# Kernel tuning notes

Measured on AMD Instinct MI355X. Metric: run time of the kernel, lower is better.

## Reference

```python
import jax, jax.numpy as jnp
import numpy as np

EPS = 1e-5

def _ln(x, g, b):
    mu = jnp.mean(x, axis=-1, keepdims=True)
    var = jnp.mean((x - mu) ** 2, axis=-1, keepdims=True)
    return (x - mu) * jax.lax.rsqrt(var + EPS) * g + b

def _lin(x, W, b):
    return x @ W + b

def setup_inputs() -> dict:
    B, D_IN, H = 32768, 512, 512
    key = jax.random.key(0)
    ks = jax.random.split(key, 20)
    def W(k, din, dout):
        return jax.random.normal(k, (din, dout), jnp.float32) / np.sqrt(din)
    inp = {
        'x': jax.random.normal(ks[0], (B, D_IN), jnp.float32),
        'h_prev': jax.random.normal(ks[1], (B, H), jnp.float32),
        's_prev': jax.random.normal(ks[2], (B, H), jnp.float32),
        'W_in': W(ks[3], D_IN, H), 'b_in': jnp.zeros((H,), jnp.float32),
        'g_ln_in': jnp.ones((H,), jnp.float32), 'b_ln_in': jnp.zeros((H,), jnp.float32),
        'g_ln_r': jnp.ones((H,), jnp.float32), 'b_ln_r': jnp.zeros((H,), jnp.float32),
        'g_ln_z': jnp.ones((H,), jnp.float32), 'b_ln_z': jnp.zeros((H,), jnp.float32),
        'g_ln_h': jnp.ones((H,), jnp.float32), 'b_ln_h': jnp.zeros((H,), jnp.float32),
        'W_r': W(ks[4], H, H), 'b_r': jnp.zeros((H,), jnp.float32),
        'W_z': W(ks[5], H, H), 'b_z': jnp.zeros((H,), jnp.float32),
        'W_k': W(ks[6], H, H), 'b_k': jnp.zeros((H,), jnp.float32),
        'W_v': W(ks[7], H, H), 'b_v': jnp.zeros((H,), jnp.float32),
        'W_h': W(ks[8], H, H), 'b_h': jnp.zeros((H,), jnp.float32),
        'W_d': W(ks[9], H, H), 'b_d': jnp.zeros((H,), jnp.float32),
    }
    return inp

def reference(x, h_prev, s_prev, W_in, b_in, g_ln_in, b_ln_in,
              g_ln_r, b_ln_r, g_ln_z, b_ln_z, g_ln_h, b_ln_h,
              W_r, b_r, W_z, b_z, W_k, b_k, W_v, b_v, W_h, b_h, W_d, b_d):
    # u = LN(input_proj(x))
    u = _ln(_lin(x, W_in, b_in), g_ln_in, b_ln_in)
    r = jax.nn.sigmoid(_ln(_lin(u, W_r, b_r), g_ln_r, b_ln_r))  # computed as in original (unused downstream)
    z = jax.nn.sigmoid(_ln(_lin(u, W_z, b_z), g_ln_z, b_ln_z))
    k = _lin(u, W_k, b_k)
    v = _lin(u, W_v, b_v)
    decay = jax.nn.sigmoid(_lin(u, W_d, b_d))
    s = decay * s_prev + k * v
    c = jnp.tanh(_ln(_lin(u + s, W_h, b_h), g_ln_h, b_ln_h))
    h = (1.0 - z) * c + z * h_prev
    return (h, s)
```

## Files before the change

### kernel.cpp

```cpp
#include <hip/hip_runtime.h>

typedef __attribute__((ext_vector_type(8))) short bf16x8;
typedef __attribute__((ext_vector_type(4))) float f32x4;

#define LN_EPS 1e-5f
#define MSZ ((size_t)32768 * 512)
#define WSZ ((size_t)512 * 512)

typedef const __attribute__((address_space(1))) void* gptr_t;
typedef __attribute__((address_space(3))) void* lptr_t;

__device__ __forceinline__ float b2f(unsigned short h) {
    unsigned int u = ((unsigned int)h) << 16;
    return __uint_as_float(u);
}
__device__ __forceinline__ short f2b(float f) {
    unsigned int u = __float_as_uint(f);
    unsigned int r = (u + 0x7FFFu + ((u >> 16) & 1u)) >> 16;
    return (short)(unsigned short)r;
}
__device__ __forceinline__ float sigmoid_f(float x) {
    return 1.0f / (1.0f + __expf(-x));
}
__device__ __forceinline__ float ldS(const void* p, size_t i, int isbf) {
    return isbf ? b2f(((const unsigned short*)p)[i]) : ((const float*)p)[i];
}
__device__ __forceinline__ void ld8(const void* p, size_t i, int isbf, float* o) {
    if (isbf) {
        bf16x8 v = *(const bf16x8*)((const unsigned short*)p + i);
        #pragma unroll
        for (int j = 0; j < 8; ++j) o[j] = b2f((unsigned short)v[j]);
    } else {
        f32x4 a = *(const f32x4*)((const float*)p + i);
        f32x4 b = *(const f32x4*)((const float*)p + i + 4);
        #pragma unroll
        for (int j = 0; j < 4; ++j) { o[j] = a[j]; o[4 + j] = b[j]; }
    }
}

__global__ void detect_dtype(const unsigned int* __restrict__ ones, int* __restrict__ flag) {
    if (threadIdx.x == 0 && blockIdx.x == 0)
        *flag = (ones[0] == 0x3F803F80u) ? 1 : 0;
}

__global__ __launch_bounds__(256) void transpose6(
    const void* __restrict__ s0, const void* __restrict__ s1,
    const void* __restrict__ s2, const void* __restrict__ s3,
    const void* __restrict__ s4, const void* __restrict__ s5,
    unsigned short* __restrict__ d0, unsigned short* __restrict__ d1,
    unsigned short* __restrict__ d2, unsigned short* __restrict__ d3,
    unsigned short* __restrict__ d4, unsigned short* __restrict__ d5,
    const int* __restrict__ flagp)
{
    const int isbf = *flagp;
    const void* srcs[6] = {s0, s1, s2, s3, s4, s5};
    unsigned short* dsts[6] = {d0, d1, d2, d3, d4, d5};
    const void* src = srcs[blockIdx.z];
    unsigned short* dst = dsts[blockIdx.z];

    __shared__ unsigned short tile[32][33];
    int tx = threadIdx.x, ty = threadIdx.y;
    int colbase = blockIdx.x * 32;
    int rowbase = blockIdx.y * 32;
    #pragma unroll
    for (int i = 0; i < 32; i += 8)
        tile[ty + i][tx] = (unsigned short)f2b(
            ldS(src, (size_t)(rowbase + ty + i) * 512 + colbase + tx, isbf));
    __syncthreads();
    #pragma unroll
    for (int i = 0; i < 32; i += 8)
        dst[(size_t)(colbase + ty + i) * 512 + rowbase + tx] = tile[tx][ty + i];
}

template<int OUT, bool CONV>
__global__ __launch_bounds__(512) void gemm_row(
    const void* __restrict__ Araw,
    const unsigned short* __restrict__ BT,
    const void* __restrict__ bias,
    const void* __restrict__ g0, const void* __restrict__ b0v,
    const void* __restrict__ g1, const void* __restrict__ b1v,
    const unsigned short* __restrict__ zlin,
    const void* __restrict__ h_prev,
    void* __restrict__ out,
    const int* __restrict__ flagp)
{
    const int isbf = *flagp;
    const int K = 512;
    __shared__ unsigned short smem[36864];
    unsigned short* As = smem;
    unsigned short* Bs = smem + 64 * 64;

    int t = threadIdx.x;
    int lane = t & 63;
    int wave = t >> 6;
    int wn = wave * 64;

    int b = blockIdx.x;
    int m0 = ((b & 7) * 64 + (b >> 3)) * 64;

    int lr = lane >> 3, lg = lane & 7, gsrc = lg ^ lr;
    const unsigned short* Ab = (const unsigned short*)Araw;

    size_t a_off = (size_t)(m0 + 8 * wave + lr) * K + gsrc * 8;
    size_t b_off[8];
    #pragma unroll
    for (int i = 0; i < 8; ++i)
        b_off[i] = (size_t)(64 * wave + 8 * i + lr) * K + gsrc * 8;

    int cr = t >> 3, cg = t & 7;

    int ml = lane & 15, kg = lane >> 4, sw = ml & 7;

    f32x4 acc[4][4] = {};
    const bool conv_now = CONV && !isbf;

    for (int k0 = 0; k0 < K; k0 += 64) {
        if (conv_now) {
            const float* Af = (const float*)Araw;
            size_t gi = (size_t)(m0 + cr) * K + k0 + cg * 8;
            f32x4 lo = *(const f32x4*)&Af[gi];
            f32x4 hi = *(const f32x4*)&Af[gi + 4];
            bf16x8 p;
            #pragma unroll
            for (int z = 0; z < 4; ++z) { p[z] = f2b(lo[z]); p[4 + z] = f2b(hi[z]); }
            *(bf16x8*)&As[cr * 64 + ((cg ^ (cr & 7)) * 8)] = p;
        } else {
            __builtin_amdgcn_global_load_lds(
                (gptr_t)(const void*)(Ab + a_off + k0),
                (lptr_t)(void*)(As + wave * 512), 16, 0, 0);
        }
        #pragma unroll
        for (int i = 0; i < 8; ++i)
            __builtin_amdgcn_global_load_lds(
                (gptr_t)(const void*)(BT + b_off[i] + k0),
                (lptr_t)(void*)(Bs + (wave * 8 + i) * 512), 16, 0, 0);
        __syncthreads();

        #pragma unroll
        for (int ks = 0; ks < 2; ++ks) {
            int ga = ((ks << 2) + kg) ^ sw;
            bf16x8 af[4], bfr[4];
            #pragma unroll
            for (int i = 0; i < 4; ++i)
                af[i] = *(const bf16x8*)&As[(i * 16 + ml) * 64 + ga * 8];
            #pragma unroll
            for (int j = 0; j < 4; ++j)
                bfr[j] = *(const bf16x8*)&Bs[(wn + j * 16 + ml) * 64 + ga * 8];
            #pragma unroll
            for (int i = 0; i < 4; ++i)
                #pragma unroll
                for (int j = 0; j < 4; ++j)
                    acc[i][j] = __builtin_amdgcn_mfma_f32_16x16x32_bf16(
                        af[i], bfr[j], acc[i][j], 0, 0, 0);
        }
        __syncthreads();
    }

    unsigned short* E = smem;
    int cq = lane >> 4, cl = lane & 15;
    #pragma unroll
    for (int j = 0; j < 4; ++j) {
        float bv = ldS(bias, wn + j * 16 + cl, isbf);
        #pragma unroll
        for (int i = 0; i < 4; ++i)
            #pragma unroll
            for (int r = 0; r < 4; ++r)
                E[(i * 16 + cq * 4 + r) * 520 + wn + j * 16 + cl] =
                    (unsigned short)f2b(acc[i][j][r] + bv);
    }
    __syncthreads();

    if (OUT == 0) {
        float gv[8], bv[8];
        ld8(g0, (size_t)lane * 8, isbf, gv);
        ld8(b0v, (size_t)lane * 8, isbf, bv);
        #pragma unroll
        for (int q = 0; q < 8; ++q) {
            int r = wave * 8 + q;
            bf16x8 xv = *(const bf16x8*)&E[r * 520 + lane * 8];
            float x[8], s = 0.f, s2 = 0.f;
            #pragma unroll
            for (int i = 0; i < 8; ++i) {
                x[i] = b2f((unsigned short)xv[i]);
                s += x[i]; s2 += x[i] * x[i];
            }
            #pragma unroll
            for (int off = 32; off > 0; off >>= 1) {
                s += __shfl_xor(s, off); s2 += __shfl_xor(s2, off);
            }
            float mu = s * (1.f / 512.f);
            float rs = rsqrtf(s2 * (1.f / 512.f) - mu * mu + LN_EPS);
            bf16x8 o;
            #pragma unroll
            for (int i = 0; i < 8; ++i)
                o[i] = f2b((x[i] - mu) * rs * gv[i] + bv[i]);
            *(bf16x8*)&((unsigned short*)out)[(size_t)(m0 + r) * 512 + lane * 8] = o;
        }
    } else {
        float gh[8], bh[8], gz[8], bz[8];
        ld8(g0, (size_t)lane * 8, isbf, gh);
        ld8(b0v, (size_t)lane * 8, isbf, bh);
        ld8(g1, (size_t)lane * 8, isbf, gz);
        ld8(b1v, (size_t)lane * 8, isbf, bz);
        #pragma unroll
        for (int q = 0; q < 8; ++q) {
            int r = wave * 8 + q;
            size_t base = (size_t)(m0 + r) * 512 + lane * 8;
            bf16x8 hv8 = *(const bf16x8*)&E[r * 520 + lane * 8];
            bf16x8 zv8 = *(const bf16x8*)&zlin[base];
            float hf[8], zf[8];
            float sh = 0.f, sh2 = 0.f, sz = 0.f, sz2 = 0.f;
            #pragma unroll
            for (int i = 0; i < 8; ++i) {
                hf[i] = b2f((unsigned short)hv8[i]);
                zf[i] = b2f((unsigned short)zv8[i]);
                sh += hf[i]; sh2 += hf[i] * hf[i];
                sz += zf[i]; sz2 += zf[i] * zf[i];
            }
            #pragma unroll
            for (int off = 32; off > 0; off >>= 1) {
                sh += __shfl_xor(sh, off); sh2 += __shfl_xor(sh2, off);
                sz += __shfl_xor(sz, off); sz2 += __shfl_xor(sz2, off);
            }
            float muh = sh * (1.f / 512.f);
            float rsh = rsqrtf(sh2 * (1.f / 512.f) - muh * muh + LN_EPS);
            float muz = sz * (1.f / 512.f);
            float rsz = rsqrtf(sz2 * (1.f / 512.f) - muz * muz + LN_EPS);
            float hp[8];
            ld8(h_prev, base, isbf, hp);
            float hout[8];
            #pragma unroll
            for (int i = 0; i < 8; ++i) {
                float z = sigmoid_f((zf[i] - muz) * rsz * gz[i] + bz[i]);
                float c = tanhf((hf[i] - muh) * rsh * gh[i] + bh[i]);
                hout[i] = (1.f - z) * c + z * hp[i];
            }
            if (isbf) {
                bf16x8 o;
                #pragma unroll
                for (int i = 0; i < 8; ++i) o[i] = f2b(hout[i]);
                *(bf16x8*)&((unsigned short*)out)[base] = o;
            } else {
                f32x4 lo, hi;
                #pragma unroll
                for (int i = 0; i < 4; ++i) { lo[i] = hout[i]; hi[i] = hout[4 + i]; }
                *(f32x4*)&((float*)out)[base] = lo;
                *(f32x4*)&((float*)out)[base + 4] = hi;
            }
        }
    }
}

__global__ __launch_bounds__(256) void gemm_zkvd(
    const unsigned short* __restrict__ U,
    const unsigned short* __restrict__ BT,
    const void* __restrict__ bz, const void* __restrict__ bk,
    const void* __restrict__ bv_, const void* __restrict__ bd,
    const void* __restrict__ s_prev,
    unsigned short* __restrict__ zout,
    unsigned short* __restrict__ aout,
    void* __restrict__ dout,
    const int* __restrict__ flagp)
{
    const int isbf = *flagp;
    const int K = 512;
    __shared__ unsigned short smem[20480];
    unsigned short* As = smem;

    int t = threadIdx.x;
    int lane = t & 63;
    int wave = t >> 6;
    int wm = (wave >> 1) * 32;
    int wn = (wave & 1) * 32;

    int b = blockIdx.x;
    int xcd = b & 7;
    int bi = b >> 3;
    int nb = bi & 7;
    int mi = bi >> 3;
    int m0 = (xcd * 64 + mi) * 64;
    int nc0 = nb * 64;

    int lr = lane >> 3, lg = lane & 7, gsrc = lg ^ lr;

    size_t a_off[2], b_off[8];
    #pragma unroll
    for (int i = 0; i < 2; ++i)
        a_off[i] = (size_t)(m0 + 8 * (2 * wave + i) + lr) * K + gsrc * 8;
    #pragma unroll
    for (int i = 0; i < 8; ++i)
        b_off[i] = (size_t)(wave * 512 + nc0 + 8 * i + lr) * K + gsrc * 8;

    int ml = lane & 15, kg = lane >> 4, sw = ml & 7;

    f32x4 acc[4][2][2] = {};

    for (int k0 = 0; k0 < K; k0 += 64) {
        #pragma unroll
        for (int i = 0; i < 2; ++i)
            __builtin_amdgcn_global_load_lds(
                (gptr_t)(const void*)(U + a_off[i] + k0),
                (lptr_t)(void*)(As + (2 * wave + i) * 512), 16, 0, 0);
        #pragma unroll
        for (int i = 0; i < 8; ++i)
            __builtin_amdgcn_global_load_lds(
                (gptr_t)(const void*)(BT + b_off[i] + k0),
                (lptr_t)(void*)(smem + 4096 + wave * 4096 + i * 512), 16, 0, 0);
        __syncthreads();

        #pragma unroll
        for (int ks = 0; ks < 2; ++ks) {
            int ga = ((ks << 2) + kg) ^ sw;
            bf16x8 af[2];
            #pragma unroll
            for (int i = 0; i < 2; ++i)
                af[i] = *(const bf16x8*)&As[(wm + i * 16 + ml) * 64 + ga * 8];
            #pragma unroll
            for (int s = 0; s < 4; ++s) {
                bf16x8 bf0 = *(const bf16x8*)&smem[4096 + s * 4096 + (wn + ml) * 64 + ga * 8];
                bf16x8 bf1 = *(const bf16x8*)&smem[4096 + s * 4096 + (wn + 16 + ml) * 64 + ga * 8];
                #pragma unroll
                for (int i = 0; i < 2; ++i) {
                    acc[s][i][0] = __builtin_amdgcn_mfma_f32_16x16x32_bf16(
                        af[i], bf0, acc[s][i][0], 0, 0, 0);
                    acc[s][i][1] = __builtin_amdgcn_mfma_f32_16x16x32_bf16(
                        af[i], bf1, acc[s][i][1], 0, 0, 0);
                }
            }
        }
        __syncthreads();
    }

    int cq = lane >> 4, cl = lane & 15;
    const void* biases[4] = {bz, bk, bv_, bd};
    #pragma unroll
    for (int s = 0; s < 4; ++s) {
        #pragma unroll
        for (int j = 0; j < 2; ++j) {
            float bvv = ldS(biases[s], nc0 + wn + j * 16 + cl, isbf);
            #pragma unroll
            for (int i = 0; i < 2; ++i)
                #pragma unroll
                for (int r = 0; r < 4; ++r)
                    smem[s * 4608 + (wm + i * 16 + cq * 4 + r) * 72 + wn + j * 16 + cl] =
                        (unsigned short)f2b(acc[s][i][j][r] + bvv);
        }
    }
    __syncthreads();

    int r = t >> 2;
    int c0 = (t & 3) * 16;
    #pragma unroll
    for (int g = 0; g < 2; ++g) {
        int col = c0 + g * 8;
        size_t idx = (size_t)(m0 + r) * 512 + nc0 + col;
        bf16x8 z8 = *(const bf16x8*)&smem[0 * 4608 + r * 72 + col];
        bf16x8 k8 = *(const bf16x8*)&smem[1 * 4608 + r * 72 + col];
        bf16x8 v8 = *(const bf16x8*)&smem[2 * 4608 + r * 72 + col];
        bf16x8 d8 = *(const bf16x8*)&smem[3 * 4608 + r * 72 + col];
        bf16x8 u8 = *(const bf16x8*)&U[idx];
        float sp[8];
        ld8(s_prev, idx, isbf, sp);
        float sv[8];
        bf16x8 a8;
        #pragma unroll
        for (int z = 0; z < 8; ++z) {
            float dv = sigmoid_f(b2f((unsigned short)d8[z]));
            sv[z] = dv * sp[z] + b2f((unsigned short)k8[z]) * b2f((unsigned short)v8[z]);
            a8[z] = f2b(b2f((unsigned short)u8[z]) + sv[z]);
        }
        *(bf16x8*)&zout[idx] = z8;
        *(bf16x8*)&aout[idx] = a8;
        if (isbf) {
            bf16x8 s8;
            #pragma unroll
            for (int z = 0; z < 8; ++z) s8[z] = f2b(sv[z]);
            *(bf16x8*)&((unsigned short*)dout)[MSZ + idx] = s8;
        } else {
            f32x4 lo, hi;
            #pragma unroll
            for (int z = 0; z < 4; ++z) { lo[z] = sv[z]; hi[z] = sv[4 + z]; }
            *(f32x4*)&((float*)dout)[MSZ + idx] = lo;
            *(f32x4*)&((float*)dout)[MSZ + idx + 4] = hi;
        }
    }
}

extern "C" void kernel_launch(void* const* d_in, const int* in_sizes, int n_in,
                              void* d_out, int out_size, void* d_ws, size_t ws_size,
                              hipStream_t stream)
{
    (void)in_sizes; (void)n_in; (void)out_size; (void)ws_size;

    const void* x       = d_in[0];
    const void* h_prev  = d_in[1];
    const void* s_prev  = d_in[2];
    const void* W_in    = d_in[3];
    const void* b_in    = d_in[4];
    const void* g_ln_in = d_in[5];
    const void* b_ln_in = d_in[6];
    const void* g_ln_z  = d_in[9];
    const void* b_ln_z  = d_in[10];
    const void* g_ln_h  = d_in[11];
    const void* b_ln_h  = d_in[12];
    const void* W_z     = d_in[15];
    const void* b_z     = d_in[16];
    const void* W_k     = d_in[17];
    const void* b_k     = d_in[18];
    const void* W_v     = d_in[19];
    const void* b_v     = d_in[20];
    const void* W_h     = d_in[21];
    const void* b_h     = d_in[22];
    const void* W_d     = d_in[23];
    const void* b_d     = d_in[24];

    unsigned short* ws = (unsigned short*)d_ws;
    unsigned short* U  = ws;
    unsigned short* L  = ws + MSZ;
    unsigned short* Ab = ws + 2 * MSZ;
    unsigned short* WT = ws + 3 * MSZ;
    unsigned short* WT_in = WT;
    unsigned short* WT_z  = WT + 1 * WSZ;
    unsigned short* WT_k  = WT + 2 * WSZ;
    unsigned short* WT_v  = WT + 3 * WSZ;
    unsigned short* WT_d  = WT + 4 * WSZ;
    unsigned short* WT_h  = WT + 5 * WSZ;
    int* flag = (int*)(WT + 6 * WSZ);
    (void)WT_k; (void)WT_v; (void)WT_d;

    detect_dtype<<<1, 64, 0, stream>>>((const unsigned int*)g_ln_in, flag);
    transpose6<<<dim3(16, 16, 6), dim3(32, 8), 0, stream>>>(
        W_in, W_z, W_k, W_v, W_d, W_h,
        WT_in, WT_z, WT_k, WT_v, WT_d, WT_h, flag);

    gemm_row<0, true><<<512, 512, 0, stream>>>(
        x, WT_in, b_in, g_ln_in, b_ln_in,
        nullptr, nullptr, nullptr, nullptr, U, flag);

    gemm_zkvd<<<4096, 256, 0, stream>>>(
        U, WT_z, b_z, b_k, b_v, b_d,
        s_prev, L, Ab, d_out, flag);

    gemm_row<1, false><<<512, 512, 0, stream>>>(
        Ab, WT_h, b_h, g_ln_h, b_ln_h,
        g_ln_z, b_ln_z, L, h_prev, d_out, flag);
}
```

Measured before the change: 458.0 us.

## Double-buffer LDS tiles in both GEMM kernels to overlap loads with MFMA

Both GEMM kernels now use two LDS buffers and prefetch the next K-tile while computing on the current one, with one barrier per iteration instead of two. gemm_row also halves its K-tile to 32 so the doubled buffers fit in LDS, and changes the swizzle and load mapping to match. gemm_zkvd doubles its LDS to 80KB, which may reduce occupancy. The aim is to hide global-to-LDS load latency behind the MFMA work.

```diff
diff --git a/kernel.cpp b/kernel.cpp
--- a/kernel.cpp
+++ b/kernel.cpp
@@ -86,9 +86,10 @@
 {
     const int isbf = *flagp;
     const int K = 512;
-    __shared__ unsigned short smem[36864];
-    unsigned short* As = smem;
-    unsigned short* Bs = smem + 64 * 64;
+    const int BK = 32;
+    const int NT = K / BK;
+    const int BUF = 18432;
+    __shared__ unsigned short smem[2 * 18432];
 
     int t = threadIdx.x;
     int lane = t & 63;
@@ -98,61 +99,70 @@
     int b = blockIdx.x;
     int m0 = ((b & 7) * 64 + (b >> 3)) * 64;
 
-    int lr = lane >> 3, lg = lane & 7, gsrc = lg ^ lr;
+    int lr = lane >> 2, lg = lane & 3;
+    int gsrc = lg ^ (lr & 3);
     const unsigned short* Ab = (const unsigned short*)Araw;
 
-    size_t a_off = (size_t)(m0 + 8 * wave + lr) * K + gsrc * 8;
-    size_t b_off[8];
-    #pragma unroll
-    for (int i = 0; i < 8; ++i)
-        b_off[i] = (size_t)(64 * wave + 8 * i + lr) * K + gsrc * 8;
-
-    int cr = t >> 3, cg = t & 7;
-
-    int ml = lane & 15, kg = lane >> 4, sw = ml & 7;
-
+    size_t b_off[4];
+    #pragma unroll
+    for (int i = 0; i < 4; ++i)
+        b_off[i] = (size_t)(64 * wave + 16 * i + lr) * K + gsrc * 8;
+    size_t a_off = (size_t)(m0 + 16 * wave + lr) * K + gsrc * 8;
+
+    int ml = lane & 15, kg = lane >> 4;
+
+    const bool conv_now = CONV && !isbf;
     f32x4 acc[4][4] = {};
-    const bool conv_now = CONV && !isbf;
-
-    for (int k0 = 0; k0 < K; k0 += 64) {
+
+    auto STAGE = [&](int co, int k0) {
         if (conv_now) {
-            const float* Af = (const float*)Araw;
-            size_t gi = (size_t)(m0 + cr) * K + k0 + cg * 8;
-            f32x4 lo = *(const f32x4*)&Af[gi];
-            f32x4 hi = *(const f32x4*)&Af[gi + 4];
-            bf16x8 p;
-            #pragma unroll
-            for (int z = 0; z < 4; ++z) { p[z] = f2b(lo[z]); p[4 + z] = f2b(hi[z]); }
-            *(bf16x8*)&As[cr * 64 + ((cg ^ (cr & 7)) * 8)] = p;
+            if (t < 256) {
+                int row = t >> 2, cg = t & 3;
+                const float* Af = (const float*)Araw;
+                size_t gi = (size_t)(m0 + row) * K + k0 + ((cg ^ (row & 3)) * 8);
+                f32x4 lo = *(const f32x4*)&Af[gi];
+                f32x4 hi = *(const f32x4*)&Af[gi + 4];
+                bf16x8 p;
+                #pragma unroll
+                for (int z = 0; z < 4; ++z) { p[z] = f2b(lo[z]); p[4 + z] = f2b(hi[z]); }
+                *(bf16x8*)&smem[co + row * 32 + cg * 8] = p;
+            }
         } else {
-            __builtin_amdgcn_global_load_lds(
-                (gptr_t)(const void*)(Ab + a_off + k0),
-                (lptr_t)(void*)(As + wave * 512), 16, 0, 0);
-        }
-        #pragma unroll
-        for (int i = 0; i < 8; ++i)
+            if (wave < 4)
+                __builtin_amdgcn_global_load_lds(
+                    (gptr_t)(const void*)(Ab + a_off + k0),
+                    (lptr_t)(void*)(smem + co + 16 * wave * 32), 16, 0, 0);
+        }
+        #pragma unroll
+        for (int i = 0; i < 4; ++i)
             __builtin_amdgcn_global_load_lds(
                 (gptr_t)(const void*)(BT + b_off[i] + k0),
-                (lptr_t)(void*)(Bs + (wave * 8 + i) * 512), 16, 0, 0);
-        __syncthreads();
-
-        #pragma unroll
-        for (int ks = 0; ks < 2; ++ks) {
-            int ga = ((ks << 2) + kg) ^ sw;
-            bf16x8 af[4], bfr[4];
-            #pragma unroll
-            for (int i = 0; i < 4; ++i)
-                af[i] = *(const bf16x8*)&As[(i * 16 + ml) * 64 + ga * 8];
+                (lptr_t)(void*)(smem + co + 2048 + (64 * wave + 16 * i) * 32), 16, 0, 0);
+    };
+
+    STAGE(0, 0);
+    __syncthreads();
+
+    for (int it = 0; it < NT; ++it) {
+        int co = (it & 1) * BUF;
+        int cn = co ^ BUF;
+        if (it + 1 < NT) STAGE(cn, (it + 1) * BK);
+
+        int gslot = kg ^ (ml & 3);
+        bf16x8 af[4], bfr[4];
+        #pragma unroll
+        for (int i = 0; i < 4; ++i)
+            af[i] = *(const bf16x8*)&smem[co + (i * 16 + ml) * 32 + gslot * 8];
+        #pragma unroll
+        for (int j = 0; j < 4; ++j)
+            bfr[j] = *(const bf16x8*)&smem[co + 2048 + (wn + j * 16 + ml) * 32 + gslot * 8];
+        #pragma unroll
+        for (int i = 0; i < 4; ++i)
             #pragma unroll
             for (int j = 0; j < 4; ++j)
-                bfr[j] = *(const bf16x8*)&Bs[(wn + j * 16 + ml) * 64 + ga * 8];
-            #pragma unroll
-            for (int i = 0; i < 4; ++i)
-                #pragma unroll
-                for (int j = 0; j < 4; ++j)
-                    acc[i][j] = __builtin_amdgcn_mfma_f32_16x16x32_bf16(
-                        af[i], bfr[j], acc[i][j], 0, 0, 0);
-        }
+                acc[i][j] = __builtin_amdgcn_mfma_f32_16x16x32_bf16(
+                    af[i], bfr[j], acc[i][j], 0, 0, 0);
+
         __syncthreads();
     }
 
@@ -264,8 +274,10 @@
 {
     const int isbf = *flagp;
     const int K = 512;
-    __shared__ unsigned short smem[20480];
-    unsigned short* As = smem;
+    const int BK = 64;
+    const int NT = K / BK;
+    const int BUF = 20480;
+    __shared__ unsigned short smem[2 * 20480];
 
     int t = threadIdx.x;
     int lane = t & 63;
@@ -295,18 +307,26 @@
 
     f32x4 acc[4][2][2] = {};
 
-    for (int k0 = 0; k0 < K; k0 += 64) {
+    auto STAGE = [&](int co, int k0) {
         #pragma unroll
         for (int i = 0; i < 2; ++i)
             __builtin_amdgcn_global_load_lds(
                 (gptr_t)(const void*)(U + a_off[i] + k0),
-                (lptr_t)(void*)(As + (2 * wave + i) * 512), 16, 0, 0);
+                (lptr_t)(void*)(smem + co + (2 * wave + i) * 512), 16, 0, 0);
         #pragma unroll
         for (int i = 0; i < 8; ++i)
             __builtin_amdgcn_global_load_lds(
                 (gptr_t)(const void*)(BT + b_off[i] + k0),
-                (lptr_t)(void*)(smem + 4096 + wave * 4096 + i * 512), 16, 0, 0);
-        __syncthreads();
+                (lptr_t)(void*)(smem + co + 4096 + wave * 4096 + i * 512), 16, 0, 0);
+    };
+
+    STAGE(0, 0);
+    __syncthreads();
+
+    for (int it = 0; it < NT; ++it) {
+        int co = (it & 1) * BUF;
+        int cn = co ^ BUF;
+        if (it + 1 < NT) STAGE(cn, (it + 1) * BK);
 
         #pragma unroll
         for (int ks = 0; ks < 2; ++ks) {
@@ -314,11 +334,11 @@
             bf16x8 af[2];
             #pragma unroll
             for (int i = 0; i < 2; ++i)
-                af[i] = *(const bf16x8*)&As[(wm + i * 16 + ml) * 64 + ga * 8];
+                af[i] = *(const bf16x8*)&smem[co + (wm + i * 16 + ml) * 64 + ga * 8];
             #pragma unroll
             for (int s = 0; s < 4; ++s) {
-                bf16x8 bf0 = *(const bf16x8*)&smem[4096 + s * 4096 + (wn + ml) * 64 + ga * 8];
-                bf16x8 bf1 = *(const bf16x8*)&smem[4096 + s * 4096 + (wn + 16 + ml) * 64 + ga * 8];
+                bf16x8 bf0 = *(const bf16x8*)&smem[co + 4096 + s * 4096 + (wn + ml) * 64 + ga * 8];
+                bf16x8 bf1 = *(const bf16x8*)&smem[co + 4096 + s * 4096 + (wn + 16 + ml) * 64 + ga * 8];
                 #pragma unroll
                 for (int i = 0; i < 2; ++i) {
                     acc[s][i][0] = __builtin_amdgcn_mfma_f32_16x16x32_bf16(
```

Result: slower. 496.4 us (+8.4%).

## Split full-row GEMM+LN kernels into 64x64-tile GEMMs plus separate LN kernels

Applied to the files above, without the earlier changes.

Replaces the full-row (64x512) GEMM kernels that fused layernorm and the output gating with a 64x64-tiled GEMM that writes bf16 intermediates. Separate row-wise kernels then apply the input layernorm and the final z/h layernorm, sigmoid, tanh and blend. The aim is more, smaller blocks with lower LDS use, for better occupancy and load balance. In exchange it adds extra global round-trips of two 32768x512 bf16 intermediates, two more kernel launches, and more A-tile reloads across column tiles.

```diff
diff --git a/kernel.cpp b/kernel.cpp
--- a/kernel.cpp
+++ b/kernel.cpp
@@ -72,182 +72,121 @@
         dst[(size_t)(colbase + ty + i) * 512 + rowbase + tx] = tile[tx][ty + i];
 }
 
-template<int OUT, bool CONV>
-__global__ __launch_bounds__(512) void gemm_row(
+template<bool CONV>
+__global__ __launch_bounds__(256) void gemm64(
     const void* __restrict__ Araw,
     const unsigned short* __restrict__ BT,
     const void* __restrict__ bias,
-    const void* __restrict__ g0, const void* __restrict__ b0v,
-    const void* __restrict__ g1, const void* __restrict__ b1v,
-    const unsigned short* __restrict__ zlin,
-    const void* __restrict__ h_prev,
-    void* __restrict__ out,
+    unsigned short* __restrict__ C,
     const int* __restrict__ flagp)
 {
     const int isbf = *flagp;
     const int K = 512;
-    __shared__ unsigned short smem[36864];
-    unsigned short* As = smem;
-    unsigned short* Bs = smem + 64 * 64;
+    __shared__ unsigned short smem[8192];
 
     int t = threadIdx.x;
     int lane = t & 63;
     int wave = t >> 6;
-    int wn = wave * 64;
+    int wm = (wave >> 1) * 32;
+    int wn = (wave & 1) * 32;
 
     int b = blockIdx.x;
-    int m0 = ((b & 7) * 64 + (b >> 3)) * 64;
+    int xcd = b & 7;
+    int bi = b >> 3;
+    int nb = bi & 7;
+    int mi = bi >> 3;
+    int m0 = (xcd * 64 + mi) * 64;
+    int n0 = nb * 64;
 
     int lr = lane >> 3, lg = lane & 7, gsrc = lg ^ lr;
     const unsigned short* Ab = (const unsigned short*)Araw;
 
-    size_t a_off = (size_t)(m0 + 8 * wave + lr) * K + gsrc * 8;
-    size_t b_off[8];
-    #pragma unroll
-    for (int i = 0; i < 8; ++i)
-        b_off[i] = (size_t)(64 * wave + 8 * i + lr) * K + gsrc * 8;
-
-    int cr = t >> 3, cg = t & 7;
+    size_t a_off[2], b_off[2];
+    #pragma unroll
+    for (int i = 0; i < 2; ++i) {
+        int c = 2 * wave + i;
+        a_off[i] = (size_t)(m0 + 8 * c + lr) * K + gsrc * 8;
+        b_off[i] = (size_t)(n0 + 8 * c + lr) * K + gsrc * 8;
+    }
 
     int ml = lane & 15, kg = lane >> 4, sw = ml & 7;
 
-    f32x4 acc[4][4] = {};
+    f32x4 acc[2][2] = {};
     const bool conv_now = CONV && !isbf;
 
     for (int k0 = 0; k0 < K; k0 += 64) {
         if (conv_now) {
             const float* Af = (const float*)Araw;
-            size_t gi = (size_t)(m0 + cr) * K + k0 + cg * 8;
-            f32x4 lo = *(const f32x4*)&Af[gi];
-            f32x4 hi = *(const f32x4*)&Af[gi + 4];
-            bf16x8 p;
-            #pragma unroll
-            for (int z = 0; z < 4; ++z) { p[z] = f2b(lo[z]); p[4 + z] = f2b(hi[z]); }
-            *(bf16x8*)&As[cr * 64 + ((cg ^ (cr & 7)) * 8)] = p;
+            int row = t >> 2;
+            #pragma unroll
+            for (int j = 0; j < 2; ++j) {
+                int G = (t & 3) * 2 + j;
+                size_t gi = (size_t)(m0 + row) * K + k0 + ((G ^ (row & 7)) * 8);
+                f32x4 lo = *(const f32x4*)&Af[gi];
+                f32x4 hi = *(const f32x4*)&Af[gi + 4];
+                bf16x8 p;
+                #pragma unroll
+                for (int z = 0; z < 4; ++z) { p[z] = f2b(lo[z]); p[4 + z] = f2b(hi[z]); }
+                *(bf16x8*)&smem[row * 64 + G * 8] = p;
+            }
         } else {
-            __builtin_amdgcn_global_load_lds(
-                (gptr_t)(const void*)(Ab + a_off + k0),
-                (lptr_t)(void*)(As + wave * 512), 16, 0, 0);
-        }
-        #pragma unroll
-        for (int i = 0; i < 8; ++i)
+            #pragma unroll
+            for (int i = 0; i < 2; ++i) {
+                int c = 2 * wave + i;
+                __builtin_amdgcn_global_load_lds(
+                    (gptr_t)(const void*)(Ab + a_off[i] + k0),
+                    (lptr_t)(void*)(smem + c * 512), 16, 0, 0);
+            }
+        }
+        #pragma unroll
+        for (int i = 0; i < 2; ++i) {
+            int c = 2 * wave + i;
             __builtin_amdgcn_global_load_lds(
                 (gptr_t)(const void*)(BT + b_off[i] + k0),
-                (lptr_t)(void*)(Bs + (wave * 8 + i) * 512), 16, 0, 0);
+                (lptr_t)(void*)(smem + 4096 + c * 512), 16, 0, 0);
+        }
         __syncthreads();
 
         #pragma unroll
         for (int ks = 0; ks < 2; ++ks) {
             int ga = ((ks << 2) + kg) ^ sw;
-            bf16x8 af[4], bfr[4];
-            #pragma unroll
-            for (int i = 0; i < 4; ++i)
-                af[i] = *(const bf16x8*)&As[(i * 16 + ml) * 64 + ga * 8];
-            #pragma unroll
-            for (int j = 0; j < 4; ++j)
-                bfr[j] = *(const bf16x8*)&Bs[(wn + j * 16 + ml) * 64 + ga * 8];
-            #pragma unroll
-            for (int i = 0; i < 4; ++i)
+            bf16x8 af[2], bfr[2];
+            #pragma unroll
+            for (int i = 0; i < 2; ++i)
+                af[i] = *(const bf16x8*)&smem[(wm + i * 16 + ml) * 64 + ga * 8];
+            #pragma unroll
+            for (int j = 0; j < 2; ++j)
+                bfr[j] = *(const bf16x8*)&smem[4096 + (wn + j * 16 + ml) * 64 + ga * 8];
+            #pragma unroll
+            for (int i = 0; i < 2; ++i)
                 #pragma unroll
-                for (int j = 0; j < 4; ++j)
+                for (int j = 0; j < 2; ++j)
                     acc[i][j] = __builtin_amdgcn_mfma_f32_16x16x32_bf16(
                         af[i], bfr[j], acc[i][j], 0, 0, 0);
         }
         __syncthreads();
     }
 
-    unsigned short* E = smem;
     int cq = lane >> 4, cl = lane & 15;
     #pragma unroll
-    for (int j = 0; j < 4; ++j) {
-        float bv = ldS(bias, wn + j * 16 + cl, isbf);
-        #pragma unroll
-        for (int i = 0; i < 4; ++i)
+    for (int j = 0; j < 2; ++j) {
+        float bv = ldS(bias, n0 + wn + j * 16 + cl, isbf);
+        #pragma unroll
+        for (int i = 0; i < 2; ++i)
             #pragma unroll
             for (int r = 0; r < 4; ++r)
-                E[(i * 16 + cq * 4 + r) * 520 + wn + j * 16 + cl] =
+                smem[(wm + i * 16 + cq * 4 + r) * 72 + wn + j * 16 + cl] =
                     (unsigned short)f2b(acc[i][j][r] + bv);
     }
     __syncthreads();
 
-    if (OUT == 0) {
-        float gv[8], bv[8];
-        ld8(g0, (size_t)lane * 8, isbf, gv);
-        ld8(b0v, (size_t)lane * 8, isbf, bv);
-        #pragma unroll
-        for (int q = 0; q < 8; ++q) {
-            int r = wave * 8 + q;
-            bf16x8 xv = *(const bf16x8*)&E[r * 520 + lane * 8];
-            float x[8], s = 0.f, s2 = 0.f;
-            #pragma unroll
-            for (int i = 0; i < 8; ++i) {
-                x[i] = b2f((unsigned short)xv[i]);
-                s += x[i]; s2 += x[i] * x[i];
-            }
-            #pragma unroll
-            for (int off = 32; off > 0; off >>= 1) {
-                s += __shfl_xor(s, off); s2 += __shfl_xor(s2, off);
-            }
-            float mu = s * (1.f / 512.f);
-            float rs = rsqrtf(s2 * (1.f / 512.f) - mu * mu + LN_EPS);
-            bf16x8 o;
-            #pragma unroll
-            for (int i = 0; i < 8; ++i)
-                o[i] = f2b((x[i] - mu) * rs * gv[i] + bv[i]);
-            *(bf16x8*)&((unsigned short*)out)[(size_t)(m0 + r) * 512 + lane * 8] = o;
-        }
-    } else {
-        float gh[8], bh[8], gz[8], bz[8];
-        ld8(g0, (size_t)lane * 8, isbf, gh);
-        ld8(b0v, (size_t)lane * 8, isbf, bh);
-        ld8(g1, (size_t)lane * 8, isbf, gz);
-        ld8(b1v, (size_t)lane * 8, isbf, bz);
-        #pragma unroll
-        for (int q = 0; q < 8; ++q) {
-            int r = wave * 8 + q;
-            size_t base = (size_t)(m0 + r) * 512 + lane * 8;
-            bf16x8 hv8 = *(const bf16x8*)&E[r * 520 + lane * 8];
-            bf16x8 zv8 = *(const bf16x8*)&zlin[base];
-            float hf[8], zf[8];
-            float sh = 0.f, sh2 = 0.f, sz = 0.f, sz2 = 0.f;
-            #pragma unroll
-            for (int i = 0; i < 8; ++i) {
-                hf[i] = b2f((unsigned short)hv8[i]);
-                zf[i] = b2f((unsigned short)zv8[i]);
-                sh += hf[i]; sh2 += hf[i] * hf[i];
-                sz += zf[i]; sz2 += zf[i] * zf[i];
-            }
-            #pragma unroll
-            for (int off = 32; off > 0; off >>= 1) {
-                sh += __shfl_xor(sh, off); sh2 += __shfl_xor(sh2, off);
-                sz += __shfl_xor(sz, off); sz2 += __shfl_xor(sz2, off);
-            }
-            float muh = sh * (1.f / 512.f);
-            float rsh = rsqrtf(sh2 * (1.f / 512.f) - muh * muh + LN_EPS);
-            float muz = sz * (1.f / 512.f);
-            float rsz = rsqrtf(sz2 * (1.f / 512.f) - muz * muz + LN_EPS);
-            float hp[8];
-            ld8(h_prev, base, isbf, hp);
-            float hout[8];
-            #pragma unroll
-            for (int i = 0; i < 8; ++i) {
-                float z = sigmoid_f((zf[i] - muz) * rsz * gz[i] + bz[i]);
-                float c = tanhf((hf[i] - muh) * rsh * gh[i] + bh[i]);
-                hout[i] = (1.f - z) * c + z * hp[i];
-            }
-            if (isbf) {
-                bf16x8 o;
-                #pragma unroll
-                for (int i = 0; i < 8; ++i) o[i] = f2b(hout[i]);
-                *(bf16x8*)&((unsigned short*)out)[base] = o;
-            } else {
-                f32x4 lo, hi;
-                #pragma unroll
-                for (int i = 0; i < 4; ++i) { lo[i] = hout[i]; hi[i] = hout[4 + i]; }
-                *(f32x4*)&((float*)out)[base] = lo;
-                *(f32x4*)&((float*)out)[base + 4] = hi;
-            }
-        }
+    int r = t >> 2;
+    int c0 = (t & 3) * 16;
+    #pragma unroll
+    for (int g = 0; g < 2; ++g) {
+        int col = c0 + g * 8;
+        *(bf16x8*)&C[(size_t)(m0 + r) * 512 + n0 + col] =
+            *(bf16x8*)&smem[r * 72 + col];
     }
 }
 
@@ -383,6 +322,108 @@
             *(f32x4*)&((float*)dout)[MSZ + idx] = lo;
             *(f32x4*)&((float*)dout)[MSZ + idx + 4] = hi;
         }
+    }
+}
+
+__global__ __launch_bounds__(256) void ln_rows(
+    const unsigned short* __restrict__ X,
+    const void* __restrict__ g,
+    const void* __restrict__ b,
+    unsigned short* __restrict__ Y,
+    const int* __restrict__ flagp)
+{
+    const int isbf = *flagp;
+    int wave = threadIdx.x >> 6, lane = threadIdx.x & 63;
+    size_t row = (size_t)blockIdx.x * 4 + wave;
+    size_t base = row * 512 + (size_t)lane * 8;
+
+    bf16x8 xv = *(const bf16x8*)&X[base];
+    float x[8];
+    float s = 0.f, s2 = 0.f;
+    #pragma unroll
+    for (int i = 0; i < 8; ++i) {
+        x[i] = b2f((unsigned short)xv[i]);
+        s += x[i]; s2 += x[i] * x[i];
+    }
+    #pragma unroll
+    for (int off = 32; off > 0; off >>= 1) {
+        s  += __shfl_xor(s, off);
+        s2 += __shfl_xor(s2, off);
+    }
+    float mu = s * (1.f / 512.f);
+    float var = s2 * (1.f / 512.f) - mu * mu;
+    float rs = rsqrtf(var + LN_EPS);
+
+    float gv[8], bv[8];
+    ld8(g, (size_t)lane * 8, isbf, gv);
+    ld8(b, (size_t)lane * 8, isbf, bv);
+    bf16x8 o;
+    #pragma unroll
+    for (int i = 0; i < 8; ++i)
+        o[i] = f2b((x[i] - mu) * rs * gv[i] + bv[i]);
+    *(bf16x8*)&Y[base] = o;
+}
+
+__global__ __launch_bounds__(256) void fused_out(
+    const unsigned short* __restrict__ hlin,
+    const unsigned short* __restrict__ zlin,
+    const void* __restrict__ h_prev,
+    const void* __restrict__ g_z, const void* __restrict__ b_z,
+    const void* __restrict__ g_h, const void* __restrict__ b_h,
+    void* __restrict__ dout,
+    const int* __restrict__ flagp)
+{
+    const int isbf = *flagp;
+    int wave = threadIdx.x >> 6, lane = threadIdx.x & 63;
+    size_t row = (size_t)blockIdx.x * 4 + wave;
+    size_t base = row * 512 + (size_t)lane * 8;
+
+    bf16x8 zv8 = *(const bf16x8*)&zlin[base];
+    bf16x8 hv8 = *(const bf16x8*)&hlin[base];
+    float zf[8], hf[8];
+    float sz = 0.f, sz2 = 0.f, sh = 0.f, sh2 = 0.f;
+    #pragma unroll
+    for (int i = 0; i < 8; ++i) {
+        zf[i] = b2f((unsigned short)zv8[i]);
+        hf[i] = b2f((unsigned short)hv8[i]);
+        sz += zf[i]; sz2 += zf[i] * zf[i];
+        sh += hf[i]; sh2 += hf[i] * hf[i];
+    }
+    #pragma unroll
+    for (int off = 32; off > 0; off >>= 1) {
+        sz  += __shfl_xor(sz, off);  sz2 += __shfl_xor(sz2, off);
+        sh  += __shfl_xor(sh, off);  sh2 += __shfl_xor(sh2, off);
+    }
+    float muz = sz * (1.f / 512.f);
+    float rsz = rsqrtf(sz2 * (1.f / 512.f) - muz * muz + LN_EPS);
+    float muh = sh * (1.f / 512.f);
+    float rsh = rsqrtf(sh2 * (1.f / 512.f) - muh * muh + LN_EPS);
+
+    float gz[8], bz[8], gh[8], bh[8], hp[8];
+    ld8(g_z, (size_t)lane * 8, isbf, gz);
+    ld8(b_z, (size_t)lane * 8, isbf, bz);
+    ld8(g_h, (size_t)lane * 8, isbf, gh);
+    ld8(b_h, (size_t)lane * 8, isbf, bh);
+    ld8(h_prev, base, isbf, hp);
+
+    float hout[8];
+    #pragma unroll
+    for (int i = 0; i < 8; ++i) {
+        float z = sigmoid_f((zf[i] - muz) * rsz * gz[i] + bz[i]);
+        float c = tanhf((hf[i] - muh) * rsh * gh[i] + bh[i]);
+        hout[i] = (1.f - z) * c + z * hp[i];
+    }
+    if (isbf) {
+        bf16x8 o;
+        #pragma unroll
+        for (int i = 0; i < 8; ++i) o[i] = f2b(hout[i]);
+        *(bf16x8*)&((unsigned short*)dout)[base] = o;
+    } else {
+        f32x4 a, b;
+        #pragma unroll
+        for (int i = 0; i < 4; ++i) { a[i] = hout[i]; b[i] = hout[4 + i]; }
+        *(f32x4*)&((float*)dout)[base] = a;
+        *(f32x4*)&((float*)dout)[base + 4] = b;
     }
 }
 
@@ -418,7 +459,8 @@
     unsigned short* U  = ws;
     unsigned short* L  = ws + MSZ;
     unsigned short* Ab = ws + 2 * MSZ;
-    unsigned short* WT = ws + 3 * MSZ;
+    unsigned short* Kb = ws + 3 * MSZ;
+    unsigned short* WT = ws + 4 * MSZ;
     unsigned short* WT_in = WT;
     unsigned short* WT_z  = WT + 1 * WSZ;
     unsigned short* WT_k  = WT + 2 * WSZ;
@@ -433,15 +475,17 @@
         W_in, W_z, W_k, W_v, W_d, W_h,
         WT_in, WT_z, WT_k, WT_v, WT_d, WT_h, flag);
 
-    gemm_row<0, true><<<512, 512, 0, stream>>>(
-        x, WT_in, b_in, g_ln_in, b_ln_in,
-        nullptr, nullptr, nullptr, nullptr, U, flag);
+    gemm64<true><<<4096, 256, 0, stream>>>(x, WT_in, b_in, L, flag);
+
+    ln_rows<<<8192, 256, 0, stream>>>(L, g_ln_in, b_ln_in, U, flag);
 
     gemm_zkvd<<<4096, 256, 0, stream>>>(
         U, WT_z, b_z, b_k, b_v, b_d,
         s_prev, L, Ab, d_out, flag);
 
-    gemm_row<1, false><<<512, 512, 0, stream>>>(
-        Ab, WT_h, b_h, g_ln_h, b_ln_h,
-        g_ln_z, b_ln_z, L, h_prev, d_out, flag);
-}
+    gemm64<false><<<4096, 256, 0, stream>>>(Ab, WT_h, b_h, Kb, flag);
+
+    fused_out<<<8192, 256, 0, stream>>>(Kb, L, h_prev,
+                                        g_ln_z, b_ln_z, g_ln_h, b_ln_h,
+                                        d_out, flag);
+}
```

After: 512.7 us. 1.12x slower.
